# Performance work log

Hardware: AMD Instinct MI355X
Metric: run time of the kernel (lower is better)

## Reference

```python
import jax, jax.numpy as jnp
import numpy as np

NUM_GROUPS = 32
EPS = 1e-6


def setup_inputs() -> dict:
    key = jax.random.key(0)
    ks = jax.random.split(key, 11)
    B, C, L = 4, 256, 4096
    s = 1.0 / np.sqrt(C)
    return {
        "x": jax.random.normal(ks[0], (B, C, L), dtype=jnp.float32),
        "gn_w": jnp.ones((C,), dtype=jnp.float32),
        "gn_b": jnp.zeros((C,), dtype=jnp.float32),
        "qw": jax.random.normal(ks[1], (C, C), dtype=jnp.float32) * s,
        "qb": jnp.zeros((C,), dtype=jnp.float32),
        "kw": jax.random.normal(ks[2], (C, C), dtype=jnp.float32) * s,
        "kb": jnp.zeros((C,), dtype=jnp.float32),
        "vw": jax.random.normal(ks[3], (C, C), dtype=jnp.float32) * s,
        "vb": jnp.zeros((C,), dtype=jnp.float32),
        "pw": jax.random.normal(ks[4], (C, C), dtype=jnp.float32) * s,
        "pb": jnp.zeros((C,), dtype=jnp.float32),
    }


def group_norm(x, w, b):
    # x: [B, C, L]; normalize over (C//G, L) within each of G=32 groups
    B, C, L = x.shape
    xg = x.reshape(B, NUM_GROUPS, (C // NUM_GROUPS) * L)
    mean = jnp.mean(xg, axis=2, keepdims=True)
    var = jnp.var(xg, axis=2, keepdims=True)
    xn = ((xg - mean) * jax.lax.rsqrt(var + EPS)).reshape(B, C, L)
    return xn * w[None, :, None] + b[None, :, None]


def conv1x1(x, w, b):
    # 1x1 Conv1d == channel matmul: [O,C] x [B,C,L] -> [B,O,L]
    return jnp.einsum('oc,bcl->bol', w, x) + b[None, :, None]


def reference(x, gn_w, gn_b, qw, qb, kw, kb, vw, vb, pw, pb):
    B, C, L = x.shape
    scale = C ** (-0.5)
    xn = group_norm(x, gn_w, gn_b)
    q = conv1x1(xn, qw, qb)
    k = conv1x1(xn, kw, kb)
    v = conv1x1(xn, vw, vb)
    attn = jnp.einsum('bci,bcj->bij', q, k) * scale  # [B, L, L]
    attn = jax.nn.softmax(attn, axis=2)
    out = jnp.einsum('bij,bcj->bci', attn, v)  # [B, C, L]
    out = conv1x1(out, pw, pb)
    return x + out
```

## Files before the change

### kernel.cpp

```cpp
#include <hip/hip_runtime.h>
#include <hip/hip_bf16.h>

#define B_ 4
#define C_ 256
#define L_ 4096
#define G_ 32
#define KVS_ 4

typedef __attribute__((ext_vector_type(8))) short bf16x8;
typedef __attribute__((ext_vector_type(4))) float f32x4;
typedef __attribute__((ext_vector_type(16))) float f32x16;
typedef __attribute__((ext_vector_type(4))) unsigned short us4;
typedef __attribute__((ext_vector_type(8))) unsigned short us8;
typedef __attribute__((ext_vector_type(4))) unsigned int u32x4;

__device__ __forceinline__ unsigned short f2bf(float f) {
  unsigned u = __builtin_bit_cast(unsigned, f);
  u += 0x7fffu + ((u >> 16) & 1u);
  return (unsigned short)(u >> 16);
}
__device__ __forceinline__ float bf2f(unsigned short s) {
  return __builtin_bit_cast(float, (unsigned)s << 16);
}

__device__ __forceinline__ void async_copy16(const void* g, void* l) {
  __builtin_amdgcn_global_load_lds((const __attribute__((address_space(1))) void*)g,
                                   (__attribute__((address_space(3))) void*)l, 16, 0, 0);
}

__global__ void wcvt_kernel(const float* __restrict__ qw, const float* __restrict__ kw,
                            const float* __restrict__ vw, const float* __restrict__ pw,
                            unsigned short* __restrict__ dst) {
  int m = blockIdx.x >> 6;
  const float* src = (m == 0) ? qw : ((m == 1) ? kw : ((m == 2) ? vw : pw));
  int i = ((blockIdx.x & 63) * 256 + threadIdx.x) * 4;
  float4 v = *(const float4*)(src + i);
  us4 o;
  o[0] = f2bf(v.x); o[1] = f2bf(v.y); o[2] = f2bf(v.z); o[3] = f2bf(v.w);
  *(us4*)(dst + m * C_ * C_ + i) = o;
}

__global__ void gn_stats_kernel(const float* __restrict__ x, float2* __restrict__ stats) {
  int bg = blockIdx.x;
  const float* xp = x + (size_t)bg * 8 * L_;
  float s = 0.f, ss = 0.f;
  for (int i = threadIdx.x * 4; i < 8 * L_; i += 1024) {
    float4 v = *(const float4*)(xp + i);
    s += v.x + v.y + v.z + v.w;
    ss += v.x * v.x + v.y * v.y + v.z * v.z + v.w * v.w;
  }
#pragma unroll
  for (int m = 1; m < 64; m <<= 1) { s += __shfl_xor(s, m); ss += __shfl_xor(ss, m); }
  __shared__ float red[8];
  int w = threadIdx.x >> 6;
  if ((threadIdx.x & 63) == 0) { red[w] = s; red[4 + w] = ss; }
  __syncthreads();
  if (threadIdx.x == 0) {
    s = red[0] + red[1] + red[2] + red[3];
    ss = red[4] + red[5] + red[6] + red[7];
    const float inv_n = 1.f / (8.f * L_);
    float mean = s * inv_n;
    float var = ss * inv_n - mean * mean;
    stats[bg] = make_float2(mean, rsqrtf(var + 1e-6f));
  }
}

__global__ void gn_apply_kernel(const float* __restrict__ x, const float* __restrict__ gw,
                                const float* __restrict__ gb, const float2* __restrict__ stats,
                                unsigned short* __restrict__ xn_t) {
  int bi = blockIdx.x;
  int b = bi >> 7, g = (bi >> 2) & 31, lc = bi & 3;
  int l = lc * 1024 + threadIdx.x * 4;
  float2 st = stats[b * 32 + g];
  float res[4][8];
#pragma unroll
  for (int j = 0; j < 8; ++j) {
    int c = g * 8 + j;
    float sw = gw[c] * st.y;
    float sb = gb[c] - st.x * sw;
    float4 v = *(const float4*)(x + ((size_t)b * C_ + c) * L_ + l);
    res[0][j] = v.x * sw + sb; res[1][j] = v.y * sw + sb;
    res[2][j] = v.z * sw + sb; res[3][j] = v.w * sw + sb;
  }
#pragma unroll
  for (int i = 0; i < 4; ++i) {
    us8 o;
#pragma unroll
    for (int j = 0; j < 8; ++j) o[j] = f2bf(res[i][j]);
    *(us8*)(xn_t + ((size_t)b * L_ + l + i) * C_ + g * 8) = o;
  }
}

__global__ __launch_bounds__(256) void qkv_gemm_kernel(
    const unsigned short* __restrict__ wq, const unsigned short* __restrict__ wk,
    const unsigned short* __restrict__ wv, const float* __restrict__ qbias,
    const float* __restrict__ kbias, const float* __restrict__ vbias,
    const unsigned short* __restrict__ xn, unsigned short* __restrict__ qt,
    unsigned short* __restrict__ kt, unsigned short* __restrict__ vt) {
  int id = blockIdx.x;
  int nt = id & 63, mt = (id >> 6) & 3, b = (id >> 8) & 3;
  int lane = threadIdx.x & 63, wid = threadIdx.x >> 6;
  int ln = lane & 15, lq = lane >> 4;
  int m0 = mt * 64 + wid * 16;
  int n0 = nt * 64;
  const unsigned short* xb = xn + (size_t)b * L_ * C_;
  bf16x8 aq[8], ak[8], av[8];
  const unsigned short* arow = wq + (m0 + ln) * C_ + lq * 8;
#pragma unroll
  for (int ks = 0; ks < 8; ++ks) aq[ks] = *(const bf16x8*)(arow + ks * 32);
  arow = wk + (m0 + ln) * C_ + lq * 8;
#pragma unroll
  for (int ks = 0; ks < 8; ++ks) ak[ks] = *(const bf16x8*)(arow + ks * 32);
  arow = wv + (m0 + ln) * C_ + lq * 8;
#pragma unroll
  for (int ks = 0; ks < 8; ++ks) av[ks] = *(const bf16x8*)(arow + ks * 32);

  int o0 = m0 + lq * 4;
  float bq[4], bk[4], bv[4];
#pragma unroll
  for (int r = 0; r < 4; ++r) { bq[r] = qbias[o0 + r]; bk[r] = kbias[o0 + r]; bv[r] = vbias[o0 + r]; }
  unsigned short* qd = qt + (size_t)b * L_ * C_;
  unsigned short* kd = kt + (size_t)b * L_ * C_;
  unsigned short* vd = vt + (size_t)b * C_ * L_;

#pragma unroll
  for (int t = 0; t < 4; ++t) {
    f32x4 cq = {0.f, 0.f, 0.f, 0.f}, ck = cq, cv = cq;
    const unsigned short* brow = xb + (size_t)(n0 + 16 * t + ln) * C_ + lq * 8;
#pragma unroll
    for (int ks = 0; ks < 8; ++ks) {
      bf16x8 bf = *(const bf16x8*)(brow + ks * 32);
      cq = __builtin_amdgcn_mfma_f32_16x16x32_bf16(aq[ks], bf, cq, 0, 0, 0);
      ck = __builtin_amdgcn_mfma_f32_16x16x32_bf16(ak[ks], bf, ck, 0, 0, 0);
      cv = __builtin_amdgcn_mfma_f32_16x16x32_bf16(av[ks], bf, cv, 0, 0, 0);
    }
    int l = n0 + 16 * t + ln;
    us4 pk;
#pragma unroll
    for (int r = 0; r < 4; ++r) pk[r] = f2bf((cq[r] + bq[r]) * 0.0625f);
    *(us4*)(qd + (size_t)l * C_ + o0) = pk;
#pragma unroll
    for (int r = 0; r < 4; ++r) pk[r] = f2bf(ck[r] + bk[r]);
    *(us4*)(kd + (size_t)l * C_ + o0) = pk;
#pragma unroll
    for (int r = 0; r < 4; ++r) vd[(size_t)(o0 + r) * L_ + l] = f2bf(cv[r] + bv[r]);
  }
}

__global__ __launch_bounds__(512) void attn_kernel(
    const unsigned short* __restrict__ qt, const unsigned short* __restrict__ kt,
    const unsigned short* __restrict__ vt, unsigned short* __restrict__ po,
    float2* __restrict__ ml) {
  __shared__ __attribute__((aligned(16))) char Kl[2][16384];
  __shared__ __attribute__((aligned(16))) char Vl[2][16384];

  int idx = (blockIdx.x & 7) * 32 + (blockIdx.x >> 3);
  int g = idx >> 4;
  int qtile = idx & 15;
  int b = g >> 2, s = g & 3;
  int jbase = s * (L_ / KVS_);
  const int NIT = (L_ / KVS_) / 32;

  int tid = threadIdx.x;
  int lane = tid & 63, wid = tid >> 6;
  int lq = lane & 31;
  int lk = lane >> 5;
  int q0 = qtile * 256 + wid * 32;

  const unsigned short* qb_ = qt + (size_t)b * L_ * C_;
  const unsigned short* kb_ = kt + (size_t)b * L_ * C_;
  const unsigned short* vb_ = vt + (size_t)b * C_ * L_;

  auto stage = [&](int j0, int bs) {
#pragma unroll
    for (int r = 0; r < 2; ++r) {
      int addr = r * 8192 + tid * 16;
      int row = addr >> 9, colb = addr & 511;
      async_copy16((const char*)kb_ + (size_t)(j0 + row) * 512 + (colb ^ ((row & 7) << 4)),
                   Kl[bs] + addr);
    }
#pragma unroll
    for (int r = 0; r < 2; ++r) {
      int addr = r * 8192 + tid * 16;
      int c = addr >> 6, colb = addr & 63;
      async_copy16((const char*)vb_ + (size_t)c * (L_ * 2) + (size_t)j0 * 2 +
                       (colb ^ (((c >> 1) & 3) << 4)),
                   Vl[bs] + addr);
    }
  };

  bf16x8 qf[16];
  const unsigned short* qrow = qb_ + (size_t)(q0 + lq) * C_ + lk * 8;
#pragma unroll
  for (int kc = 0; kc < 16; ++kc) qf[kc] = *(const bf16x8*)(qrow + kc * 16);

  stage(jbase, 0);
  stage(jbase + 32, 1);

  f32x16 oacc[8];
#pragma unroll
  for (int ct = 0; ct < 8; ++ct)
#pragma unroll
    for (int i = 0; i < 16; ++i) oacc[ct][i] = 0.f;

  float m_run = -3e38f, l_run = 0.f;
  const float LOG2E = 1.44269504f;
  const int kswz = (lq & 7) << 4;
  const int vswz = ((lq >> 1) & 3) << 4;

#pragma unroll 1
  for (int jt = 0; jt < NIT; ++jt) {
    const char* Kb = Kl[jt & 1];
    const char* Vb = Vl[jt & 1];

    asm volatile("s_waitcnt vmcnt(4)" ::: "memory");
    __builtin_amdgcn_sched_barrier(0);
    __builtin_amdgcn_s_barrier();
    __builtin_amdgcn_sched_barrier(0);

    f32x16 sa, sb;
#pragma unroll
    for (int i = 0; i < 16; ++i) { sa[i] = 0.f; sb[i] = 0.f; }
#pragma unroll
    for (int kc = 0; kc < 16; kc += 2) {
      bf16x8 kf0 = *(const bf16x8*)(Kb + lq * 512 + ((kc * 32 + lk * 16) ^ kswz));
      sa = __builtin_amdgcn_mfma_f32_32x32x16_bf16(kf0, qf[kc], sa, 0, 0, 0);
      bf16x8 kf1 = *(const bf16x8*)(Kb + lq * 512 + (((kc + 1) * 32 + lk * 16) ^ kswz));
      sb = __builtin_amdgcn_mfma_f32_32x32x16_bf16(kf1, qf[kc + 1], sb, 0, 0, 0);
    }
    f32x16 sacc = sa + sb;

    float pm = sacc[0];
#pragma unroll
    for (int i = 1; i < 16; ++i) pm = fmaxf(pm, sacc[i]);
    pm = fmaxf(pm, __shfl_xor(pm, 32));
    if (__any(pm > m_run + 8.0f)) {
      float mn = fmaxf(m_run, pm);
      float al = exp2f((m_run - mn) * LOG2E);
      l_run *= al;
#pragma unroll
      for (int ct = 0; ct < 8; ++ct)
#pragma unroll
        for (int i = 0; i < 16; ++i) oacc[ct][i] *= al;
      m_run = mn;
    }
    float p[16];
    float ls = 0.f;
#pragma unroll
    for (int i = 0; i < 16; ++i) {
      p[i] = exp2f((sacc[i] - m_run) * LOG2E);
      ls += p[i];
    }
    ls += __shfl_xor(ls, 32);
    l_run += ls;

    unsigned w[8];
#pragma unroll
    for (int i = 0; i < 8; ++i)
      asm("v_cvt_pk_bf16_f32 %0, %1, %2" : "=v"(w[i]) : "v"(p[2 * i]), "v"(p[2 * i + 1]));
    asm volatile("v_permlane32_swap_b32 %0, %1" : "+v"(w[0]), "+v"(w[2]));
    asm volatile("v_permlane32_swap_b32 %0, %1" : "+v"(w[1]), "+v"(w[3]));
    asm volatile("v_permlane32_swap_b32 %0, %1" : "+v"(w[4]), "+v"(w[6]));
    asm volatile("v_permlane32_swap_b32 %0, %1" : "+v"(w[5]), "+v"(w[7]));
    u32x4 t1 = {w[0], w[1], w[2], w[3]};
    u32x4 t2 = {w[4], w[5], w[6], w[7]};
    bf16x8 pb1 = __builtin_bit_cast(bf16x8, t1);
    bf16x8 pb2 = __builtin_bit_cast(bf16x8, t2);

#pragma unroll
    for (int ct = 0; ct < 8; ++ct) {
      int vr = ct * 32 + lq;
      bf16x8 av0 = *(const bf16x8*)(Vb + vr * 64 + ((lk * 16) ^ vswz));
      oacc[ct] = __builtin_amdgcn_mfma_f32_32x32x16_bf16(av0, pb1, oacc[ct], 0, 0, 0);
      bf16x8 av1 = *(const bf16x8*)(Vb + vr * 64 + ((32 + lk * 16) ^ vswz));
      oacc[ct] = __builtin_amdgcn_mfma_f32_32x32x16_bf16(av1, pb2, oacc[ct], 0, 0, 0);
    }

    __builtin_amdgcn_sched_barrier(0);
    __builtin_amdgcn_s_barrier();
    __builtin_amdgcn_sched_barrier(0);
    stage(jbase + ((jt + 2) & (NIT - 1)) * 32, jt & 1);
  }

  asm volatile("s_waitcnt vmcnt(0)" ::: "memory");

  unsigned short* pob = po + ((size_t)g * L_ + q0 + lq) * C_;
#pragma unroll
  for (int ct = 0; ct < 8; ++ct) {
#pragma unroll
    for (int e = 0; e < 4; ++e) {
      us4 pk;
#pragma unroll
      for (int r = 0; r < 4; ++r) pk[r] = f2bf(oacc[ct][4 * e + r]);
      *(us4*)(pob + ct * 32 + 8 * e + 4 * lk) = pk;
    }
  }
  if (lane < 32)
    ml[(size_t)g * L_ + q0 + lq] = make_float2(m_run, l_run);
}

__global__ void combine_kernel(const unsigned short* __restrict__ po,
                               const float2* __restrict__ ml,
                               unsigned short* __restrict__ ot) {
  int tid = threadIdx.x;
  int row = blockIdx.x * 4 + (tid >> 6);
  int b = row >> 12;
  int l = row & (L_ - 1);
  int lane = tid & 63;
  const float LOG2E = 1.44269504f;
  float2 mv[KVS_];
  float M = -3e38f;
#pragma unroll
  for (int s = 0; s < KVS_; ++s) {
    mv[s] = ml[(size_t)(b * KVS_ + s) * L_ + l];
    M = fmaxf(M, mv[s].x);
  }
  float acc[4] = {0.f, 0.f, 0.f, 0.f};
  float denom = 0.f;
#pragma unroll
  for (int s = 0; s < KVS_; ++s) {
    float w = exp2f((mv[s].x - M) * LOG2E);
    denom += w * mv[s].y;
    us4 o = *(const us4*)(po + ((size_t)(b * KVS_ + s) * L_ + l) * C_ + lane * 4);
#pragma unroll
    for (int j = 0; j < 4; ++j) acc[j] += w * bf2f(o[j]);
  }
  float inv = 1.f / denom;
  us4 o;
#pragma unroll
  for (int j = 0; j < 4; ++j) o[j] = f2bf(acc[j] * inv);
  *(us4*)(ot + (size_t)row * C_ + lane * 4) = o;
}

__global__ __launch_bounds__(256) void proj_kernel(
    const unsigned short* __restrict__ wp, const float* __restrict__ pbias,
    const unsigned short* __restrict__ ot, const float* __restrict__ x,
    float* __restrict__ out) {
  int id = blockIdx.x;
  int nt = id & 63, mt = (id >> 6) & 3, b = id >> 8;
  int lane = threadIdx.x & 63, wid = threadIdx.x >> 6;
  int ln = lane & 15, lq = lane >> 4;
  int m0 = mt * 64 + wid * 16;
  int n0 = nt * 64;
  const unsigned short* ob = ot + (size_t)b * L_ * C_;
  bf16x8 a[8];
  const unsigned short* arow = wp + (m0 + ln) * C_ + lq * 8;
#pragma unroll
  for (int ks = 0; ks < 8; ++ks) a[ks] = *(const bf16x8*)(arow + ks * 32);
  f32x4 acc[4];
#pragma unroll
  for (int t = 0; t < 4; ++t) {
    f32x4 c = {0.f, 0.f, 0.f, 0.f};
    const unsigned short* brow = ob + (size_t)(n0 + 16 * t + ln) * C_ + lq * 8;
#pragma unroll
    for (int ks = 0; ks < 8; ++ks) {
      bf16x8 bf = *(const bf16x8*)(brow + ks * 32);
      c = __builtin_amdgcn_mfma_f32_16x16x32_bf16(a[ks], bf, c, 0, 0, 0);
    }
    acc[t] = c;
  }
  int o0 = m0 + lq * 4;
#pragma unroll
  for (int r = 0; r < 4; ++r) {
    float bvr = pbias[o0 + r];
    const float* xrow = x + ((size_t)b * C_ + o0 + r) * L_;
    float* orow = out + ((size_t)b * C_ + o0 + r) * L_;
#pragma unroll
    for (int t = 0; t < 4; ++t) {
      int l = n0 + 16 * t + ln;
      orow[l] = xrow[l] + acc[t][r] + bvr;
    }
  }
}

extern "C" void kernel_launch(void* const* d_in, const int* in_sizes, int n_in,
                              void* d_out, int out_size, void* d_ws, size_t ws_size,
                              hipStream_t stream) {
  const float* x   = (const float*)d_in[0];
  const float* gnw = (const float*)d_in[1];
  const float* gnb = (const float*)d_in[2];
  const float* qw  = (const float*)d_in[3];
  const float* qb  = (const float*)d_in[4];
  const float* kw  = (const float*)d_in[5];
  const float* kb  = (const float*)d_in[6];
  const float* vw  = (const float*)d_in[7];
  const float* vb  = (const float*)d_in[8];
  const float* pw  = (const float*)d_in[9];
  const float* pb  = (const float*)d_in[10];
  float* out = (float*)d_out;

  unsigned short* ws = (unsigned short*)d_ws;
  const size_t SZ = (size_t)B_ * L_ * C_;
  unsigned short* xn_t = ws;
  unsigned short* qt   = xn_t + SZ;
  unsigned short* kt   = qt + SZ;
  unsigned short* vt   = kt + SZ;
  unsigned short* ot   = vt + SZ;
  unsigned short* wb   = ot + SZ;
  float2* stats = (float2*)(wb + 4 * C_ * C_);
  unsigned short* po = (unsigned short*)(stats + B_ * G_);
  float2* ml = (float2*)(po + (size_t)KVS_ * SZ);

  wcvt_kernel<<<256, 256, 0, stream>>>(qw, kw, vw, pw, wb);
  gn_stats_kernel<<<B_ * G_, 256, 0, stream>>>(x, stats);
  gn_apply_kernel<<<512, 256, 0, stream>>>(x, gnw, gnb, stats, xn_t);
  qkv_gemm_kernel<<<1024, 256, 0, stream>>>(wb, wb + C_ * C_, wb + 2 * C_ * C_,
                                            qb, kb, vb, xn_t, qt, kt, vt);
  attn_kernel<<<256, 512, 0, stream>>>(qt, kt, vt, po, ml);
  combine_kernel<<<B_ * L_ / 4, 256, 0, stream>>>(po, ml, ot);
  proj_kernel<<<1024, 256, 0, stream>>>(wb + 3 * C_ * C_, pb, ot, x, out);
}
```

Measured before the change: 212.4 us.

## Fuse GN kernels, convert weights inline, software-pipeline QK^T in attention

Merges the group-norm stats and apply kernels into one kernel per (batch, group). It also drops the separate weight-conversion kernel by converting fp32 weights to bf16 inside the GEMM kernels. The attention loop is restructured with a triple-buffered K tile so the QK^T MFMAs for the next tile overlap the softmax and PV work of the current tile, with s_setprio hints. This saves kernel launches at the cost of less parallelism in the GN kernel (128 blocks), redundant weight conversion per block, and more LDS and registers in attention.

```diff
diff --git a/kernel.cpp b/kernel.cpp
--- a/kernel.cpp
+++ b/kernel.cpp
@@ -28,20 +28,21 @@
                                    (__attribute__((address_space(3))) void*)l, 16, 0, 0);
 }
 
-__global__ void wcvt_kernel(const float* __restrict__ qw, const float* __restrict__ kw,
-                            const float* __restrict__ vw, const float* __restrict__ pw,
-                            unsigned short* __restrict__ dst) {
-  int m = blockIdx.x >> 6;
-  const float* src = (m == 0) ? qw : ((m == 1) ? kw : ((m == 2) ? vw : pw));
-  int i = ((blockIdx.x & 63) * 256 + threadIdx.x) * 4;
-  float4 v = *(const float4*)(src + i);
-  us4 o;
-  o[0] = f2bf(v.x); o[1] = f2bf(v.y); o[2] = f2bf(v.z); o[3] = f2bf(v.w);
-  *(us4*)(dst + m * C_ * C_ + i) = o;
-}
-
-__global__ void gn_stats_kernel(const float* __restrict__ x, float2* __restrict__ stats) {
+__device__ __forceinline__ bf16x8 ld_w8(const float* p) {
+  float4 f0 = *(const float4*)(p);
+  float4 f1 = *(const float4*)(p + 4);
+  us8 o;
+  o[0] = f2bf(f0.x); o[1] = f2bf(f0.y); o[2] = f2bf(f0.z); o[3] = f2bf(f0.w);
+  o[4] = f2bf(f1.x); o[5] = f2bf(f1.y); o[6] = f2bf(f1.z); o[7] = f2bf(f1.w);
+  return __builtin_bit_cast(bf16x8, o);
+}
+
+__global__ __launch_bounds__(256) void gn_kernel(const float* __restrict__ x,
+                                                 const float* __restrict__ gw,
+                                                 const float* __restrict__ gb,
+                                                 unsigned short* __restrict__ xn_t) {
   int bg = blockIdx.x;
+  int b = bg >> 5, g = bg & 31;
   const float* xp = x + (size_t)bg * 8 * L_;
   float s = 0.f, ss = 0.f;
   for (int i = threadIdx.x * 4; i < 8 * L_; i += 1024) {
@@ -55,45 +56,42 @@
   int w = threadIdx.x >> 6;
   if ((threadIdx.x & 63) == 0) { red[w] = s; red[4 + w] = ss; }
   __syncthreads();
-  if (threadIdx.x == 0) {
-    s = red[0] + red[1] + red[2] + red[3];
-    ss = red[4] + red[5] + red[6] + red[7];
-    const float inv_n = 1.f / (8.f * L_);
-    float mean = s * inv_n;
-    float var = ss * inv_n - mean * mean;
-    stats[bg] = make_float2(mean, rsqrtf(var + 1e-6f));
-  }
-}
-
-__global__ void gn_apply_kernel(const float* __restrict__ x, const float* __restrict__ gw,
-                                const float* __restrict__ gb, const float2* __restrict__ stats,
-                                unsigned short* __restrict__ xn_t) {
-  int bi = blockIdx.x;
-  int b = bi >> 7, g = (bi >> 2) & 31, lc = bi & 3;
-  int l = lc * 1024 + threadIdx.x * 4;
-  float2 st = stats[b * 32 + g];
-  float res[4][8];
+  s = red[0] + red[1] + red[2] + red[3];
+  ss = red[4] + red[5] + red[6] + red[7];
+  const float inv_n = 1.f / (8.f * L_);
+  float mean = s * inv_n;
+  float rstd = rsqrtf(ss * inv_n - mean * mean + 1e-6f);
+
+  float sw[8], sb[8];
 #pragma unroll
   for (int j = 0; j < 8; ++j) {
     int c = g * 8 + j;
-    float sw = gw[c] * st.y;
-    float sb = gb[c] - st.x * sw;
-    float4 v = *(const float4*)(x + ((size_t)b * C_ + c) * L_ + l);
-    res[0][j] = v.x * sw + sb; res[1][j] = v.y * sw + sb;
-    res[2][j] = v.z * sw + sb; res[3][j] = v.w * sw + sb;
-  }
-#pragma unroll
-  for (int i = 0; i < 4; ++i) {
-    us8 o;
-#pragma unroll
-    for (int j = 0; j < 8; ++j) o[j] = f2bf(res[i][j]);
-    *(us8*)(xn_t + ((size_t)b * L_ + l + i) * C_ + g * 8) = o;
+    sw[j] = gw[c] * rstd;
+    sb[j] = gb[c] - mean * sw[j];
+  }
+#pragma unroll 1
+  for (int lc = 0; lc < 4; ++lc) {
+    int l = lc * 1024 + threadIdx.x * 4;
+    float res[4][8];
+#pragma unroll
+    for (int j = 0; j < 8; ++j) {
+      float4 v = *(const float4*)(x + ((size_t)b * C_ + g * 8 + j) * L_ + l);
+      res[0][j] = v.x * sw[j] + sb[j]; res[1][j] = v.y * sw[j] + sb[j];
+      res[2][j] = v.z * sw[j] + sb[j]; res[3][j] = v.w * sw[j] + sb[j];
+    }
+#pragma unroll
+    for (int i = 0; i < 4; ++i) {
+      us8 o;
+#pragma unroll
+      for (int j = 0; j < 8; ++j) o[j] = f2bf(res[i][j]);
+      *(us8*)(xn_t + ((size_t)b * L_ + l + i) * C_ + g * 8) = o;
+    }
   }
 }
 
 __global__ __launch_bounds__(256) void qkv_gemm_kernel(
-    const unsigned short* __restrict__ wq, const unsigned short* __restrict__ wk,
-    const unsigned short* __restrict__ wv, const float* __restrict__ qbias,
+    const float* __restrict__ wq, const float* __restrict__ wk,
+    const float* __restrict__ wv, const float* __restrict__ qbias,
     const float* __restrict__ kbias, const float* __restrict__ vbias,
     const unsigned short* __restrict__ xn, unsigned short* __restrict__ qt,
     unsigned short* __restrict__ kt, unsigned short* __restrict__ vt) {
@@ -105,15 +103,12 @@
   int n0 = nt * 64;
   const unsigned short* xb = xn + (size_t)b * L_ * C_;
   bf16x8 aq[8], ak[8], av[8];
-  const unsigned short* arow = wq + (m0 + ln) * C_ + lq * 8;
-#pragma unroll
-  for (int ks = 0; ks < 8; ++ks) aq[ks] = *(const bf16x8*)(arow + ks * 32);
-  arow = wk + (m0 + ln) * C_ + lq * 8;
-#pragma unroll
-  for (int ks = 0; ks < 8; ++ks) ak[ks] = *(const bf16x8*)(arow + ks * 32);
-  arow = wv + (m0 + ln) * C_ + lq * 8;
-#pragma unroll
-  for (int ks = 0; ks < 8; ++ks) av[ks] = *(const bf16x8*)(arow + ks * 32);
+#pragma unroll
+  for (int ks = 0; ks < 8; ++ks) aq[ks] = ld_w8(wq + (m0 + ln) * C_ + lq * 8 + ks * 32);
+#pragma unroll
+  for (int ks = 0; ks < 8; ++ks) ak[ks] = ld_w8(wk + (m0 + ln) * C_ + lq * 8 + ks * 32);
+#pragma unroll
+  for (int ks = 0; ks < 8; ++ks) av[ks] = ld_w8(wv + (m0 + ln) * C_ + lq * 8 + ks * 32);
 
   int o0 = m0 + lq * 4;
   float bq[4], bk[4], bv[4];
@@ -151,7 +146,7 @@
     const unsigned short* __restrict__ qt, const unsigned short* __restrict__ kt,
     const unsigned short* __restrict__ vt, unsigned short* __restrict__ po,
     float2* __restrict__ ml) {
-  __shared__ __attribute__((aligned(16))) char Kl[2][16384];
+  __shared__ __attribute__((aligned(16))) char Kl[3][16384];
   __shared__ __attribute__((aligned(16))) char Vl[2][16384];
 
   int idx = (blockIdx.x & 7) * 32 + (blockIdx.x >> 3);
@@ -171,22 +166,28 @@
   const unsigned short* kb_ = kt + (size_t)b * L_ * C_;
   const unsigned short* vb_ = vt + (size_t)b * C_ * L_;
 
-  auto stage = [&](int j0, int bs) {
+  auto stageK = [&](int slot, int jtile) {
+    int j0 = jbase + jtile * 32;
 #pragma unroll
     for (int r = 0; r < 2; ++r) {
       int addr = r * 8192 + tid * 16;
       int row = addr >> 9, colb = addr & 511;
       async_copy16((const char*)kb_ + (size_t)(j0 + row) * 512 + (colb ^ ((row & 7) << 4)),
-                   Kl[bs] + addr);
-    }
+                   Kl[slot] + addr);
+    }
+  };
+  auto stageV = [&](int jtile) {
+    int j0 = jbase + jtile * 32;
+    char* Vb = Vl[jtile & 1];
 #pragma unroll
     for (int r = 0; r < 2; ++r) {
       int addr = r * 8192 + tid * 16;
       int c = addr >> 6, colb = addr & 63;
       async_copy16((const char*)vb_ + (size_t)c * (L_ * 2) + (size_t)j0 * 2 +
                        (colb ^ (((c >> 1) & 3) << 4)),
-                   Vl[bs] + addr);
-    }
+                   Vl[(jtile & 1)] + addr);
+    }
+    (void)Vb;
   };
 
   bf16x8 qf[16];
@@ -194,8 +195,11 @@
 #pragma unroll
   for (int kc = 0; kc < 16; ++kc) qf[kc] = *(const bf16x8*)(qrow + kc * 16);
 
-  stage(jbase, 0);
-  stage(jbase + 32, 1);
+  stageK(0, 0);
+  stageV(0);
+  stageK(1, 1);
+  stageV(1);
+  stageK(2, 2);
 
   f32x16 oacc[8];
 #pragma unroll
@@ -208,31 +212,49 @@
   const int kswz = (lq & 7) << 4;
   const int vswz = ((lq >> 1) & 3) << 4;
 
-#pragma unroll 1
-  for (int jt = 0; jt < NIT; ++jt) {
-    const char* Kb = Kl[jt & 1];
-    const char* Vb = Vl[jt & 1];
-
+  asm volatile("s_waitcnt vmcnt(8)" ::: "memory");
+  __builtin_amdgcn_sched_barrier(0);
+  __builtin_amdgcn_s_barrier();
+  __builtin_amdgcn_sched_barrier(0);
+
+  f32x16 sA, sB;
+  {
+    f32x16 t1, t2;
+#pragma unroll
+    for (int i = 0; i < 16; ++i) { t1[i] = 0.f; t2[i] = 0.f; }
+#pragma unroll
+    for (int kc = 0; kc < 16; kc += 2) {
+      bf16x8 kf0 = *(const bf16x8*)(Kl[0] + lq * 512 + ((kc * 32 + lk * 16) ^ kswz));
+      t1 = __builtin_amdgcn_mfma_f32_32x32x16_bf16(kf0, qf[kc], t1, 0, 0, 0);
+      bf16x8 kf1 = *(const bf16x8*)(Kl[0] + lq * 512 + (((kc + 1) * 32 + lk * 16) ^ kswz));
+      t2 = __builtin_amdgcn_mfma_f32_32x32x16_bf16(kf1, qf[kc + 1], t2, 0, 0, 0);
+    }
+    sA = t1 + t2;
+  }
+
+  auto body = [&](int jt, f32x16& sprev, f32x16& snext) {
     asm volatile("s_waitcnt vmcnt(4)" ::: "memory");
     __builtin_amdgcn_sched_barrier(0);
     __builtin_amdgcn_s_barrier();
     __builtin_amdgcn_sched_barrier(0);
 
-    f32x16 sa, sb;
-#pragma unroll
-    for (int i = 0; i < 16; ++i) { sa[i] = 0.f; sb[i] = 0.f; }
+    const char* Kb = Kl[(jt + 1) % 3];
+    f32x16 t1, t2;
+#pragma unroll
+    for (int i = 0; i < 16; ++i) { t1[i] = 0.f; t2[i] = 0.f; }
+    __builtin_amdgcn_s_setprio(1);
 #pragma unroll
     for (int kc = 0; kc < 16; kc += 2) {
       bf16x8 kf0 = *(const bf16x8*)(Kb + lq * 512 + ((kc * 32 + lk * 16) ^ kswz));
-      sa = __builtin_amdgcn_mfma_f32_32x32x16_bf16(kf0, qf[kc], sa, 0, 0, 0);
+      t1 = __builtin_amdgcn_mfma_f32_32x32x16_bf16(kf0, qf[kc], t1, 0, 0, 0);
       bf16x8 kf1 = *(const bf16x8*)(Kb + lq * 512 + (((kc + 1) * 32 + lk * 16) ^ kswz));
-      sb = __builtin_amdgcn_mfma_f32_32x32x16_bf16(kf1, qf[kc + 1], sb, 0, 0, 0);
-    }
-    f32x16 sacc = sa + sb;
-
-    float pm = sacc[0];
-#pragma unroll
-    for (int i = 1; i < 16; ++i) pm = fmaxf(pm, sacc[i]);
+      t2 = __builtin_amdgcn_mfma_f32_32x32x16_bf16(kf1, qf[kc + 1], t2, 0, 0, 0);
+    }
+    __builtin_amdgcn_s_setprio(0);
+
+    float pm = sprev[0];
+#pragma unroll
+    for (int i = 1; i < 16; ++i) pm = fmaxf(pm, sprev[i]);
     pm = fmaxf(pm, __shfl_xor(pm, 32));
     if (__any(pm > m_run + 8.0f)) {
       float mn = fmaxf(m_run, pm);
@@ -248,11 +270,13 @@
     float ls = 0.f;
 #pragma unroll
     for (int i = 0; i < 16; ++i) {
-      p[i] = exp2f((sacc[i] - m_run) * LOG2E);
+      p[i] = exp2f((sprev[i] - m_run) * LOG2E);
       ls += p[i];
     }
     ls += __shfl_xor(ls, 32);
     l_run += ls;
+
+    snext = t1 + t2;
 
     unsigned w[8];
 #pragma unroll
@@ -262,11 +286,13 @@
     asm volatile("v_permlane32_swap_b32 %0, %1" : "+v"(w[1]), "+v"(w[3]));
     asm volatile("v_permlane32_swap_b32 %0, %1" : "+v"(w[4]), "+v"(w[6]));
     asm volatile("v_permlane32_swap_b32 %0, %1" : "+v"(w[5]), "+v"(w[7]));
-    u32x4 t1 = {w[0], w[1], w[2], w[3]};
-    u32x4 t2 = {w[4], w[5], w[6], w[7]};
-    bf16x8 pb1 = __builtin_bit_cast(bf16x8, t1);
-    bf16x8 pb2 = __builtin_bit_cast(bf16x8, t2);
-
+    u32x4 u1 = {w[0], w[1], w[2], w[3]};
+    u32x4 u2 = {w[4], w[5], w[6], w[7]};
+    bf16x8 pb1 = __builtin_bit_cast(bf16x8, u1);
+    bf16x8 pb2 = __builtin_bit_cast(bf16x8, u2);
+
+    const char* Vb = Vl[jt & 1];
+    __builtin_amdgcn_s_setprio(1);
 #pragma unroll
     for (int ct = 0; ct < 8; ++ct) {
       int vr = ct * 32 + lq;
@@ -275,11 +301,19 @@
       bf16x8 av1 = *(const bf16x8*)(Vb + vr * 64 + ((32 + lk * 16) ^ vswz));
       oacc[ct] = __builtin_amdgcn_mfma_f32_32x32x16_bf16(av1, pb2, oacc[ct], 0, 0, 0);
     }
+    __builtin_amdgcn_s_setprio(0);
 
     __builtin_amdgcn_sched_barrier(0);
     __builtin_amdgcn_s_barrier();
     __builtin_amdgcn_sched_barrier(0);
-    stage(jbase + ((jt + 2) & (NIT - 1)) * 32, jt & 1);
+    stageK((jt + 3) % 3, (jt + 3) & (NIT - 1));
+    stageV((jt + 2) & (NIT - 1));
+  };
+
+#pragma unroll 1
+  for (int jt2 = 0; jt2 < NIT; jt2 += 2) {
+    body(jt2, sA, sB);
+    body(jt2 + 1, sB, sA);
   }
 
   asm volatile("s_waitcnt vmcnt(0)" ::: "memory");
@@ -333,7 +367,7 @@
 }
 
 __global__ __launch_bounds__(256) void proj_kernel(
-    const unsigned short* __restrict__ wp, const float* __restrict__ pbias,
+    const float* __restrict__ wp, const float* __restrict__ pbias,
     const unsigned short* __restrict__ ot, const float* __restrict__ x,
     float* __restrict__ out) {
   int id = blockIdx.x;
@@ -344,9 +378,8 @@
   int n0 = nt * 64;
   const unsigned short* ob = ot + (size_t)b * L_ * C_;
   bf16x8 a[8];
-  const unsigned short* arow = wp + (m0 + ln) * C_ + lq * 8;
-#pragma unroll
-  for (int ks = 0; ks < 8; ++ks) a[ks] = *(const bf16x8*)(arow + ks * 32);
+#pragma unroll
+  for (int ks = 0; ks < 8; ++ks) a[ks] = ld_w8(wp + (m0 + ln) * C_ + lq * 8 + ks * 32);
   f32x4 acc[4];
 #pragma unroll
   for (int t = 0; t < 4; ++t) {
@@ -396,17 +429,12 @@
   unsigned short* kt   = qt + SZ;
   unsigned short* vt   = kt + SZ;
   unsigned short* ot   = vt + SZ;
-  unsigned short* wb   = ot + SZ;
-  float2* stats = (float2*)(wb + 4 * C_ * C_);
-  unsigned short* po = (unsigned short*)(stats + B_ * G_);
+  unsigned short* po   = ot + SZ;
   float2* ml = (float2*)(po + (size_t)KVS_ * SZ);
 
-  wcvt_kernel<<<256, 256, 0, stream>>>(qw, kw, vw, pw, wb);
-  gn_stats_kernel<<<B_ * G_, 256, 0, stream>>>(x, stats);
-  gn_apply_kernel<<<512, 256, 0, stream>>>(x, gnw, gnb, stats, xn_t);
-  qkv_gemm_kernel<<<1024, 256, 0, stream>>>(wb, wb + C_ * C_, wb + 2 * C_ * C_,
-                                            qb, kb, vb, xn_t, qt, kt, vt);
+  gn_kernel<<<B_ * G_, 256, 0, stream>>>(x, gnw, gnb, xn_t);
+  qkv_gemm_kernel<<<1024, 256, 0, stream>>>(qw, kw, vw, qb, kb, vb, xn_t, qt, kt, vt);
   attn_kernel<<<256, 512, 0, stream>>>(qt, kt, vt, po, ml);
   combine_kernel<<<B_ * L_ / 4, 256, 0, stream>>>(po, ml, ot);
-  proj_kernel<<<1024, 256, 0, stream>>>(wb + 3 * C_ * C_, pb, ot, x, out);
-}
+  proj_kernel<<<1024, 256, 0, stream>>>(pw, pb, ot, x, out);
+}
```

New measurement: 444.7 us. 2.09x slower.

## Fuse GroupNorm kernels, fold log2e into Q scale, tune attention waits and priority

Applied to the files above, without the earlier changes.

Merges the GroupNorm stats and apply kernels into one kernel per (batch, group), which removes a launch and the stats round trip. It also folds log2(e) into the Q scaling so the softmax exp2 calls no longer multiply by LOG2E. In the attention loop it relaxes the vmcnt wait from 4 to 8 and raises wave priority around the MFMA sections. The fused GN runs only 128 blocks, which lowers parallelism for the apply phase.

```diff
diff --git a/kernel.cpp b/kernel.cpp
--- a/kernel.cpp
+++ b/kernel.cpp
@@ -40,8 +40,12 @@
   *(us4*)(dst + m * C_ * C_ + i) = o;
 }
 
-__global__ void gn_stats_kernel(const float* __restrict__ x, float2* __restrict__ stats) {
+__global__ __launch_bounds__(256) void gn_kernel(const float* __restrict__ x,
+                                                 const float* __restrict__ gw,
+                                                 const float* __restrict__ gb,
+                                                 unsigned short* __restrict__ xn_t) {
   int bg = blockIdx.x;
+  int b = bg >> 5, g = bg & 31;
   const float* xp = x + (size_t)bg * 8 * L_;
   float s = 0.f, ss = 0.f;
   for (int i = threadIdx.x * 4; i < 8 * L_; i += 1024) {
@@ -55,39 +59,36 @@
   int w = threadIdx.x >> 6;
   if ((threadIdx.x & 63) == 0) { red[w] = s; red[4 + w] = ss; }
   __syncthreads();
-  if (threadIdx.x == 0) {
-    s = red[0] + red[1] + red[2] + red[3];
-    ss = red[4] + red[5] + red[6] + red[7];
-    const float inv_n = 1.f / (8.f * L_);
-    float mean = s * inv_n;
-    float var = ss * inv_n - mean * mean;
-    stats[bg] = make_float2(mean, rsqrtf(var + 1e-6f));
-  }
-}
-
-__global__ void gn_apply_kernel(const float* __restrict__ x, const float* __restrict__ gw,
-                                const float* __restrict__ gb, const float2* __restrict__ stats,
-                                unsigned short* __restrict__ xn_t) {
-  int bi = blockIdx.x;
-  int b = bi >> 7, g = (bi >> 2) & 31, lc = bi & 3;
-  int l = lc * 1024 + threadIdx.x * 4;
-  float2 st = stats[b * 32 + g];
-  float res[4][8];
+  s = red[0] + red[1] + red[2] + red[3];
+  ss = red[4] + red[5] + red[6] + red[7];
+  const float inv_n = 1.f / (8.f * L_);
+  float mean = s * inv_n;
+  float rstd = rsqrtf(ss * inv_n - mean * mean + 1e-6f);
+
+  float sw[8], sb[8];
 #pragma unroll
   for (int j = 0; j < 8; ++j) {
     int c = g * 8 + j;
-    float sw = gw[c] * st.y;
-    float sb = gb[c] - st.x * sw;
-    float4 v = *(const float4*)(x + ((size_t)b * C_ + c) * L_ + l);
-    res[0][j] = v.x * sw + sb; res[1][j] = v.y * sw + sb;
-    res[2][j] = v.z * sw + sb; res[3][j] = v.w * sw + sb;
-  }
-#pragma unroll
-  for (int i = 0; i < 4; ++i) {
-    us8 o;
-#pragma unroll
-    for (int j = 0; j < 8; ++j) o[j] = f2bf(res[i][j]);
-    *(us8*)(xn_t + ((size_t)b * L_ + l + i) * C_ + g * 8) = o;
+    sw[j] = gw[c] * rstd;
+    sb[j] = gb[c] - mean * sw[j];
+  }
+#pragma unroll 1
+  for (int lc = 0; lc < 4; ++lc) {
+    int l = lc * 1024 + threadIdx.x * 4;
+    float res[4][8];
+#pragma unroll
+    for (int j = 0; j < 8; ++j) {
+      float4 v = *(const float4*)(x + ((size_t)b * C_ + g * 8 + j) * L_ + l);
+      res[0][j] = v.x * sw[j] + sb[j]; res[1][j] = v.y * sw[j] + sb[j];
+      res[2][j] = v.z * sw[j] + sb[j]; res[3][j] = v.w * sw[j] + sb[j];
+    }
+#pragma unroll
+    for (int i = 0; i < 4; ++i) {
+      us8 o;
+#pragma unroll
+      for (int j = 0; j < 8; ++j) o[j] = f2bf(res[i][j]);
+      *(us8*)(xn_t + ((size_t)b * L_ + l + i) * C_ + g * 8) = o;
+    }
   }
 }
 
@@ -122,6 +123,7 @@
   unsigned short* qd = qt + (size_t)b * L_ * C_;
   unsigned short* kd = kt + (size_t)b * L_ * C_;
   unsigned short* vd = vt + (size_t)b * C_ * L_;
+  const float QSCALE = 0.0625f * 1.44269504f;
 
 #pragma unroll
   for (int t = 0; t < 4; ++t) {
@@ -137,7 +139,7 @@
     int l = n0 + 16 * t + ln;
     us4 pk;
 #pragma unroll
-    for (int r = 0; r < 4; ++r) pk[r] = f2bf((cq[r] + bq[r]) * 0.0625f);
+    for (int r = 0; r < 4; ++r) pk[r] = f2bf((cq[r] + bq[r]) * QSCALE);
     *(us4*)(qd + (size_t)l * C_ + o0) = pk;
 #pragma unroll
     for (int r = 0; r < 4; ++r) pk[r] = f2bf(ck[r] + bk[r]);
@@ -204,7 +206,6 @@
     for (int i = 0; i < 16; ++i) oacc[ct][i] = 0.f;
 
   float m_run = -3e38f, l_run = 0.f;
-  const float LOG2E = 1.44269504f;
   const int kswz = (lq & 7) << 4;
   const int vswz = ((lq >> 1) & 3) << 4;
 
@@ -213,7 +214,7 @@
     const char* Kb = Kl[jt & 1];
     const char* Vb = Vl[jt & 1];
 
-    asm volatile("s_waitcnt vmcnt(4)" ::: "memory");
+    asm volatile("s_waitcnt vmcnt(8)" ::: "memory");
     __builtin_amdgcn_sched_barrier(0);
     __builtin_amdgcn_s_barrier();
     __builtin_amdgcn_sched_barrier(0);
@@ -221,6 +222,7 @@
     f32x16 sa, sb;
 #pragma unroll
     for (int i = 0; i < 16; ++i) { sa[i] = 0.f; sb[i] = 0.f; }
+    __builtin_amdgcn_s_setprio(1);
 #pragma unroll
     for (int kc = 0; kc < 16; kc += 2) {
       bf16x8 kf0 = *(const bf16x8*)(Kb + lq * 512 + ((kc * 32 + lk * 16) ^ kswz));
@@ -228,6 +230,7 @@
       bf16x8 kf1 = *(const bf16x8*)(Kb + lq * 512 + (((kc + 1) * 32 + lk * 16) ^ kswz));
       sb = __builtin_amdgcn_mfma_f32_32x32x16_bf16(kf1, qf[kc + 1], sb, 0, 0, 0);
     }
+    __builtin_amdgcn_s_setprio(0);
     f32x16 sacc = sa + sb;
 
     float pm = sacc[0];
@@ -236,7 +239,7 @@
     pm = fmaxf(pm, __shfl_xor(pm, 32));
     if (__any(pm > m_run + 8.0f)) {
       float mn = fmaxf(m_run, pm);
-      float al = exp2f((m_run - mn) * LOG2E);
+      float al = exp2f(m_run - mn);
       l_run *= al;
 #pragma unroll
       for (int ct = 0; ct < 8; ++ct)
@@ -248,7 +251,7 @@
     float ls = 0.f;
 #pragma unroll
     for (int i = 0; i < 16; ++i) {
-      p[i] = exp2f((sacc[i] - m_run) * LOG2E);
+      p[i] = exp2f(sacc[i] - m_run);
       ls += p[i];
     }
     ls += __shfl_xor(ls, 32);
@@ -267,6 +270,7 @@
     bf16x8 pb1 = __builtin_bit_cast(bf16x8, t1);
     bf16x8 pb2 = __builtin_bit_cast(bf16x8, t2);
 
+    __builtin_amdgcn_s_setprio(1);
 #pragma unroll
     for (int ct = 0; ct < 8; ++ct) {
       int vr = ct * 32 + lq;
@@ -275,6 +279,7 @@
       bf16x8 av1 = *(const bf16x8*)(Vb + vr * 64 + ((32 + lk * 16) ^ vswz));
       oacc[ct] = __builtin_amdgcn_mfma_f32_32x32x16_bf16(av1, pb2, oacc[ct], 0, 0, 0);
     }
+    __builtin_amdgcn_s_setprio(0);
 
     __builtin_amdgcn_sched_barrier(0);
     __builtin_amdgcn_s_barrier();
@@ -307,7 +312,6 @@
   int b = row >> 12;
   int l = row & (L_ - 1);
   int lane = tid & 63;
-  const float LOG2E = 1.44269504f;
   float2 mv[KVS_];
   float M = -3e38f;
 #pragma unroll
@@ -319,7 +323,7 @@
   float denom = 0.f;
 #pragma unroll
   for (int s = 0; s < KVS_; ++s) {
-    float w = exp2f((mv[s].x - M) * LOG2E);
+    float w = exp2f(mv[s].x - M);
     denom += w * mv[s].y;
     us4 o = *(const us4*)(po + ((size_t)(b * KVS_ + s) * L_ + l) * C_ + lane * 4);
 #pragma unroll
@@ -397,13 +401,11 @@
   unsigned short* vt   = kt + SZ;
   unsigned short* ot   = vt + SZ;
   unsigned short* wb   = ot + SZ;
-  float2* stats = (float2*)(wb + 4 * C_ * C_);
-  unsigned short* po = (unsigned short*)(stats + B_ * G_);
+  unsigned short* po   = wb + 4 * C_ * C_;
   float2* ml = (float2*)(po + (size_t)KVS_ * SZ);
 
   wcvt_kernel<<<256, 256, 0, stream>>>(qw, kw, vw, pw, wb);
-  gn_stats_kernel<<<B_ * G_, 256, 0, stream>>>(x, stats);
-  gn_apply_kernel<<<512, 256, 0, stream>>>(x, gnw, gnb, stats, xn_t);
+  gn_kernel<<<B_ * G_, 256, 0, stream>>>(x, gnw, gnb, xn_t);
   qkv_gemm_kernel<<<1024, 256, 0, stream>>>(wb, wb + C_ * C_, wb + 2 * C_ * C_,
                                             qb, kb, vb, xn_t, qt, kt, vt);
   attn_kernel<<<256, 512, 0, stream>>>(qt, kt, vt, po, ml);
```

Result: no change. 212.6 us (+0.1%).
